# Kernel tuning notes

Measured on AMD Instinct MI355X. Metric: run time of the kernel, lower is better.

The kernel has to match this reference:

```python
import jax, jax.numpy as jnp
import numpy as np
import math

H = 8          # num_heads
DH = 16        # dim_head
DEPTH = 1
LAMBDA_INIT = 0.8 - 0.6 * math.exp(-0.3 * DEPTH)
LN_EPS = 1e-5


def setup_inputs() -> dict:
    key = jax.random.key(0)
    ks = jax.random.split(key, 12)
    dim = 256
    inner = 2 * H * DH  # 256
    b, n = 2, 2048
    s = lambda fan_in: 1.0 / math.sqrt(fan_in)
    return {
        "x": jax.random.normal(ks[0], (b, n, dim), jnp.float32),
        "Wq": jax.random.normal(ks[1], (dim, inner), jnp.float32) * s(dim),
        "Wkv": jax.random.normal(ks[2], (dim, 2 * inner), jnp.float32) * s(dim),
        "Wout": jax.random.normal(ks[3], (inner, dim), jnp.float32) * s(inner),
        "bout": jnp.zeros((dim,), jnp.float32),
        "Wg": jax.random.normal(ks[4], (dim, inner), jnp.float32) * s(dim),
        "bg": jnp.ones((inner,), jnp.float32),
        "lq1": jax.random.normal(ks[5], (DH,), jnp.float32) * 0.1,
        "lk1": jax.random.normal(ks[6], (DH,), jnp.float32) * 0.1,
        "lq2": jax.random.normal(ks[7], (DH,), jnp.float32) * 0.1,
        "lk2": jax.random.normal(ks[8], (DH,), jnp.float32) * 0.1,
        "ln_gamma": jnp.ones((2 * DH,), jnp.float32),
        "ln_beta": jnp.zeros((2 * DH,), jnp.float32),
    }


def reference(x, Wq, Wkv, Wout, bout, Wg, bg, lq1, lk1, lq2, lk2, ln_gamma, ln_beta):
    b, n, dim = x.shape
    scale = DH ** (-0.5)

    q = x @ Wq                                   # [b, n, 2*H*DH]
    kv = x @ Wkv                                 # [b, n, 4*H*DH]
    k, v = jnp.split(kv, 2, axis=-1)

    # doubled heads for q, k; normal heads with width 2*DH for v
    q = q.reshape(b, n, 2 * H, DH).transpose(0, 2, 1, 3) * scale  # [b, 2H, n, DH]
    k = k.reshape(b, n, 2 * H, DH).transpose(0, 2, 1, 3)          # [b, 2H, n, DH]
    v = v.reshape(b, n, H, 2 * DH).transpose(0, 2, 1, 3)          # [b, H, n, 2DH]

    dots = jnp.einsum('bhid,bhjd->bhij', q, k)   # [b, 2H, n, n]
    attn = jax.nn.softmax(dots, axis=-1)

    lam1 = jnp.exp(jnp.sum(lq1 * lk1))
    lam2 = jnp.exp(jnp.sum(lq2 * lk2))
    lam = lam1 - lam2 + LAMBDA_INIT

    attn = attn.reshape(b, H, 2, n, n)
    attn = attn[:, :, 0] - lam * attn[:, :, 1]   # [b, H, n, n]

    out = jnp.einsum('bhij,bhjd->bhid', attn, v)  # [b, H, n, 2DH]

    # LayerNorm over last dim (2*DH)
    mu = jnp.mean(out, axis=-1, keepdims=True)
    var = jnp.var(out, axis=-1, keepdims=True)
    out = (out - mu) * jax.lax.rsqrt(var + LN_EPS) * ln_gamma + ln_beta

    out = out * (1.0 - LAMBDA_INIT)
    out = out.transpose(0, 2, 1, 3).reshape(b, n, H * 2 * DH)  # [b, n, inner]

    gates = x @ Wg + bg
    out = out * jax.nn.sigmoid(gates)
    return out @ Wout + bout
```

## Files before the change

kernel.cpp:

```cpp
#include <hip/hip_runtime.h>
#include <hip/hip_bf16.h>

#define LAMBDA_INIT_F 0.35550906759096927f
#define ONE_MINUS_LI  0.64449093240903073f
#define QSCALE 0.36067376022224085f

typedef unsigned short u16;
typedef unsigned int   u32;
typedef short s8v  __attribute__((ext_vector_type(8)));
typedef u32   u32x4 __attribute__((ext_vector_type(4)));
typedef float f16v __attribute__((ext_vector_type(16)));

__device__ __forceinline__ u16 f2bf(float f) {
    __hip_bfloat16 h = __float2bfloat16(f);
    return *reinterpret_cast<u16*>(&h);
}
__device__ __forceinline__ u32 pk2bf(float lo, float hi) {
    return (u32)f2bf(lo) | ((u32)f2bf(hi) << 16);
}
union U4S8 { u32 u[4]; s8v s; };
__device__ __forceinline__ s8v mks8(u32 a, u32 b, u32 c, u32 d) {
    U4S8 x; x.u[0]=a; x.u[1]=b; x.u[2]=c; x.u[3]=d; return x.s;
}

__device__ __forceinline__ float fexp2(float x) {
#if __has_builtin(__builtin_amdgcn_exp2f)
    return __builtin_amdgcn_exp2f(x);
#else
    float r; asm volatile("v_exp_f32 %0, %1\n\ts_nop 1" : "=v"(r) : "v"(x)); return r;
#endif
}

#define MFMA16(a,b,c) __builtin_amdgcn_mfma_f32_32x32x16_bf16((a),(b),(c),0,0,0)

__device__ __forceinline__ void plswap2(u32& a, u32& b) {
    auto r = __builtin_amdgcn_permlane32_swap(a, b, false, false);
    a = r[0]; b = r[1];
}

__global__ __launch_bounds__(256) void prep_kernel(
    const float* __restrict__ Wq, const float* __restrict__ Wkv,
    const float* __restrict__ Wg, const float* __restrict__ Wout,
    const float* __restrict__ x,
    u16* __restrict__ WT, u16* __restrict__ xbf)
{
    const int bid = blockIdx.x;
    const int tid = threadIdx.x;

    if (bid >= 80) {
        const int r0 = (bid - 80) * 64;
        const float4* src = (const float4*)(x + (size_t)r0 * 256);
        u32* dst = (u32*)(xbf + (size_t)r0 * 256);
        for (int idx = tid; idx < 64 * 64; idx += 256) {
            float4 v = src[idx];
            dst[2*idx + 0] = pk2bf(v.x, v.y);
            dst[2*idx + 1] = pk2bf(v.z, v.w);
        }
        return;
    }

    __shared__ u16 tile[16 * 258];
    const int n0g = bid * 16;
    const float* src; int cols; int ncol0;
    if      (n0g < 256)  { src = Wq;   cols = 256; ncol0 = n0g; }
    else if (n0g < 768)  { src = Wkv;  cols = 512; ncol0 = n0g - 256; }
    else if (n0g < 1024) { src = Wg;   cols = 256; ncol0 = n0g - 768; }
    else                 { src = Wout; cols = 256; ncol0 = n0g - 1024; }

    const float* srow = src + (size_t)tid * cols + ncol0;
#pragma unroll
    for (int j = 0; j < 8; ++j) {
        const float2 v = *(const float2*)(srow + 2*j);
        tile[(2*j + 0) * 258 + tid] = f2bf(v.x);
        tile[(2*j + 1) * 258 + tid] = f2bf(v.y);
    }
    __syncthreads();

    const u32* t32 = (const u32*)tile;
    const int nn = tid >> 4, part = tid & 15;
    u32* dst = (u32*)WT + (size_t)(n0g + nn) * 128 + part * 8;
    const u32* s2 = t32 + nn * 129 + part * 8;
#pragma unroll
    for (int j = 0; j < 8; ++j) dst[j] = s2[j];
}

__global__ __launch_bounds__(256) void proj_kernel(
    const u16* __restrict__ x, const u16* __restrict__ WT,
    const float* __restrict__ bg,
    u16* __restrict__ Qb, u16* __restrict__ Kb,
    u16* __restrict__ Vb, float* __restrict__ Gb)
{
    const int bid = blockIdx.x;
    const int nt = bid & 15, mt = bid >> 4;
    const int tid = threadIdx.x, w = tid >> 6, lane = tid & 63;
    const int l31 = lane & 31, hh = lane >> 5;
    const int ms = w & 1, nsub = w >> 1;
    const int m0 = mt * 64 + ms * 32;
    const int n0 = nt * 64 + nsub * 32;

    const u16* xr = x  + (size_t)(m0 + l31) * 256 + 8*hh;
    const u16* br = WT + (size_t)(n0 + l31) * 256 + 8*hh;

    f16v a0;
#pragma unroll
    for (int r = 0; r < 16; ++r) a0[r] = 0.f;

#pragma unroll
    for (int ks = 0; ks < 16; ++ks) {
        s8v xa = *(const s8v*)(xr + ks*16);
        s8v w0 = *(const s8v*)(br + ks*16);
        a0 = MFMA16(xa, w0, a0);
    }

    const int cat = nt >> 2;
    const int n = n0 + l31;
#pragma unroll
    for (int r = 0; r < 16; ++r) {
        const int il = (r & 3) + 8*(r >> 2) + 4*hh;
        const int R = m0 + il;
        const int b = R >> 11, i = R & 2047;
        const float v = a0[r];
        if (cat == 0) {
            const int h = n >> 4, d = n & 15;
            Qb[((size_t)(b*16 + h) * 2048 + i) * 16 + d] = f2bf(v * QSCALE);
        } else if (cat == 1) {
            const int nk = n - 256, h = nk >> 4, d = nk & 15;
            Kb[((size_t)(b*16 + h) * 2048 + i) * 16 + d] = f2bf(v);
        } else if (cat == 2) {
            const int nv = n - 512, hv = nv >> 5, d2 = nv & 31;
            Vb[((size_t)(b*8 + hv) * 2048 + i) * 32 + d2] = f2bf(v);
        } else {
            const int gcol = n - 768;
            const float t = v + bg[gcol];
            Gb[(size_t)R * 256 + gcol] = 1.0f / (1.0f + __expf(-t));
        }
    }
}

__global__ __launch_bounds__(512, 8) void attn_kernel(
    const u16* __restrict__ Q, const u16* __restrict__ K,
    const u16* __restrict__ V, const float* __restrict__ G,
    const float* __restrict__ lq1, const float* __restrict__ lk1,
    const float* __restrict__ lq2, const float* __restrict__ lk2,
    const float* __restrict__ gamma, const float* __restrict__ beta,
    u16* __restrict__ A)
{
    __shared__ float smemf[8960];
    u16* st  = (u16*)smemf;
    u32* stu = (u32*)smemf;

    const int bid = blockIdx.x;
    const int itile = bid & 63;
    const int combo = bid >> 6;
    const int ho = combo & 7, b = combo >> 3;
    const int i0 = itile * 32;

    const int tid = threadIdx.x, w = tid >> 6, lane = tid & 63;
    const int l31 = lane & 31, hh = lane >> 5;
    const int s = w & 1, jq = w >> 1;

    const u16* Vg = V + (size_t)(b*8 + ho) * 2048 * 32;
    const u16* Qg = Q + ((size_t)(b*16 + 2*ho + s) * 2048 + (i0 + l31)) * 16;
    const s8v qf = *(const s8v*)(Qg + 8*hh);

    const int qp = tid >> 7;
    const int pid = tid & 127;
    const int ksub = pid >> 6, krow = (pid >> 1) & 31, kseg = pid & 1;
    const u32* kgp = (const u32*)(K + (size_t)(b*16 + 2*ho + ksub) * 2048 * 16)
                     + (size_t)qp * 4096 + krow * 8 + kseg * 4;
    const int vj = pid >> 2, vseg = pid & 3;
    const u32* vgp = (const u32*)Vg + (size_t)qp * 8192 + vj * 16 + vseg * 4;

    const int kw_off = qp*1120 + ksub*288 + krow*9 + kseg*4;
    const int vw_u16 = qp*2240 + 1152 + vj;
    const int vd0 = vseg * 8;
    const int kr_off = jq*1120 + s*288 + l31*9 + 4*hh;
    const int vr_off = jq*1120 + 576 + l31*17;

    f16v oacc;
#pragma unroll
    for (int r = 0; r < 16; ++r) oacc[r] = 0.f;
    float la0 = 0.f, la1 = 0.f;

    {
        u32 k0 = kgp[0], k1 = kgp[1], k2 = kgp[2], k3 = kgp[3];
        u32 v0 = vgp[0], v1 = vgp[1], v2 = vgp[2], v3 = vgp[3];
        u32* kd = stu + kw_off;
        kd[0]=k0; kd[1]=k1; kd[2]=k2; kd[3]=k3;
        u16* vd = st + vw_u16;
        vd[(vd0+0)*34] = (u16)(v0 & 0xffff); vd[(vd0+1)*34] = (u16)(v0 >> 16);
        vd[(vd0+2)*34] = (u16)(v1 & 0xffff); vd[(vd0+3)*34] = (u16)(v1 >> 16);
        vd[(vd0+4)*34] = (u16)(v2 & 0xffff); vd[(vd0+5)*34] = (u16)(v2 >> 16);
        vd[(vd0+6)*34] = (u16)(v3 & 0xffff); vd[(vd0+7)*34] = (u16)(v3 >> 16);
    }

    for (int t = 0; t < 16; ++t) {
        __syncthreads();
        const int p = t & 1, pn = 1 - p;
        const int tt = (t + 1) & 15;

        const u32* kp = kgp + (size_t)tt * 256;
        u32 nk0=kp[0], nk1=kp[1], nk2=kp[2], nk3=kp[3];
        const u32* vp = vgp + (size_t)tt * 512;
        u32 nv0=vp[0], nv1=vp[1], nv2=vp[2], nv3=vp[3];

        const u32* kb2 = stu + p*4480 + kr_off;
        const u32* vb2 = stu + p*4480 + vr_off;

        f16v sc;
#pragma unroll
        for (int r = 0; r < 16; ++r) sc[r] = 0.f;
        {
            s8v kf = mks8(kb2[0], kb2[1], kb2[2], kb2[3]);
            sc = MFMA16(kf, qf, sc);
        }
        float pv[16];
#pragma unroll
        for (int r = 0; r < 16; ++r) pv[r] = fexp2(sc[r]);
        la0 += pv[0];  la0 += pv[1];  la0 += pv[2];  la0 += pv[3];
        la1 += pv[4];  la1 += pv[5];  la1 += pv[6];  la1 += pv[7];
        la0 += pv[8];  la0 += pv[9];  la0 += pv[10]; la0 += pv[11];
        la1 += pv[12]; la1 += pv[13]; la1 += pv[14]; la1 += pv[15];

        u32 wv[8];
#pragma unroll
        for (int i = 0; i < 8; ++i)
            wv[i] = __builtin_amdgcn_perm(__float_as_uint(pv[2*i+1]),
                                          __float_as_uint(pv[2*i+0]), 0x07060302);
        plswap2(wv[0], wv[2]); plswap2(wv[1], wv[3]);
        {
            s8v pf0 = mks8(wv[0], wv[1], wv[2], wv[3]);
            s8v vf0 = mks8(vb2[4*hh+0], vb2[4*hh+1], vb2[4*hh+2], vb2[4*hh+3]);
            oacc = MFMA16(pf0, vf0, oacc);
        }
        plswap2(wv[4], wv[6]); plswap2(wv[5], wv[7]);
        {
            s8v pf1 = mks8(wv[4], wv[5], wv[6], wv[7]);
            s8v vf1 = mks8(vb2[8+4*hh+0], vb2[8+4*hh+1], vb2[8+4*hh+2], vb2[8+4*hh+3]);
            oacc = MFMA16(pf1, vf1, oacc);
        }

        {
            u32* kd = stu + pn*4480 + kw_off;
            kd[0]=nk0; kd[1]=nk1; kd[2]=nk2; kd[3]=nk3;
            u16* vd = st + pn*8960 + vw_u16;
            vd[(vd0+0)*34] = (u16)(nv0 & 0xffff); vd[(vd0+1)*34] = (u16)(nv0 >> 16);
            vd[(vd0+2)*34] = (u16)(nv1 & 0xffff); vd[(vd0+3)*34] = (u16)(nv1 >> 16);
            vd[(vd0+4)*34] = (u16)(nv2 & 0xffff); vd[(vd0+5)*34] = (u16)(nv2 >> 16);
            vd[(vd0+6)*34] = (u16)(nv3 & 0xffff); vd[(vd0+7)*34] = (u16)(nv3 >> 16);
        }
    }
    const float lacc = la0 + la1;

    __syncthreads();
    float ltot = lacc + __shfl_xor(lacc, 32);
    float* ob = smemf + w * 1056;
#pragma unroll
    for (int r = 0; r < 16; ++r) {
        const int il = (r & 3) + 8*(r >> 2) + 4*hh;
        ob[il*33 + l31] = oacc[r];
    }
    if (lane < 32) smemf[8448 + w*32 + l31] = ltot;
    __syncthreads();

    if (tid < 128) {
        const int ii = tid >> 2, sub = tid & 3, d0 = sub * 8;
        float l1 = 0.f, l2 = 0.f;
#pragma unroll
        for (int q = 0; q < 4; ++q) {
            l1 += smemf[8448 + (2*q + 0)*32 + ii];
            l2 += smemf[8448 + (2*q + 1)*32 + ii];
        }

        float sA = 0.f, sB = 0.f;
#pragma unroll
        for (int d = 0; d < 16; ++d) {
            sA += lq1[d] * lk1[d];
            sB += lq2[d] * lk2[d];
        }
        const float lam = __expf(sA) - __expf(sB) + LAMBDA_INIT_F;
        const float c1 = 1.f / l1, c2 = lam / l2;

        float od[8]; float mu = 0.f;
#pragma unroll
        for (int dd = 0; dd < 8; ++dd) {
            const int d = d0 + dd;
            float o1 = 0.f, o2 = 0.f;
#pragma unroll
            for (int q = 0; q < 4; ++q) {
                o1 += smemf[(2*q + 0)*1056 + ii*33 + d];
                o2 += smemf[(2*q + 1)*1056 + ii*33 + d];
            }
            od[dd] = o1 * c1 - o2 * c2;
            mu += od[dd];
        }
        mu += __shfl_xor(mu, 1); mu += __shfl_xor(mu, 2);
        mu *= (1.f / 32.f);
        float var = 0.f;
#pragma unroll
        for (int dd = 0; dd < 8; ++dd) { const float t2 = od[dd] - mu; var += t2 * t2; }
        var += __shfl_xor(var, 1); var += __shfl_xor(var, 2);
        var *= (1.f / 32.f);
        const float rs = rsqrtf(var + 1e-5f);

        const int R = b*2048 + i0 + ii;
        const float* Gr = G + (size_t)R * 256 + ho*32 + d0;
        const float4 g0 = *(const float4*)(Gr);
        const float4 g1 = *(const float4*)(Gr + 4);
        const float gg[8] = { g0.x, g0.y, g0.z, g0.w, g1.x, g1.y, g1.z, g1.w };
        float vals[8];
#pragma unroll
        for (int dd = 0; dd < 8; ++dd) {
            const float val = (od[dd] - mu)*rs*gamma[d0 + dd] + beta[d0 + dd];
            vals[dd] = val * ONE_MINUS_LI * gg[dd];
        }
        u32x4 pk;
        pk[0] = pk2bf(vals[0], vals[1]);
        pk[1] = pk2bf(vals[2], vals[3]);
        pk[2] = pk2bf(vals[4], vals[5]);
        pk[3] = pk2bf(vals[6], vals[7]);
        *reinterpret_cast<u32x4*>(A + (size_t)R * 256 + ho*32 + d0) = pk;
    }
}

__global__ __launch_bounds__(512) void out_kernel(
    const u16* __restrict__ Abf, const u16* __restrict__ WT,
    const float* __restrict__ bout, float* __restrict__ out)
{
    __shared__ float cs[4][32 * 33];

    const int bid = blockIdx.x;
    const int nt = bid & 3, mt = bid >> 2;
    const int tid = threadIdx.x, w = tid >> 6, lane = tid & 63;
    const int l31 = lane & 31, hh = lane >> 5;
    const int t = w >> 1, kh = w & 1;
    const int m0 = mt * 64 + (t & 1) * 32;
    const int n0 = nt * 64 + (t >> 1) * 32;

    const u16* ar = Abf + (size_t)(m0 + l31) * 256 + kh*128 + 8*hh;
    const u16* br = WT + (size_t)(1024 + n0 + l31) * 256 + kh*128 + 8*hh;

    f16v acc;
#pragma unroll
    for (int r = 0; r < 16; ++r) acc[r] = 0.f;

#pragma unroll
    for (int ks = 0; ks < 8; ++ks) {
        s8v aa = *(const s8v*)(ar + ks*16);
        s8v ba = *(const s8v*)(br + ks*16);
        acc = MFMA16(aa, ba, acc);
    }

    if (kh == 0) {
#pragma unroll
        for (int r = 0; r < 16; ++r) {
            const int il = (r & 3) + 8*(r >> 2) + 4*hh;
            cs[t][il*33 + l31] = acc[r];
        }
    }
    __syncthreads();
    if (kh == 1) {
        const float bv = bout[n0 + l31];
#pragma unroll
        for (int r = 0; r < 16; ++r) {
            const int il = (r & 3) + 8*(r >> 2) + 4*hh;
            const int m = m0 + il;
            out[(size_t)m * 256 + n0 + l31] = acc[r] + cs[t][il*33 + l31] + bv;
        }
    }
}

extern "C" void kernel_launch(void* const* d_in, const int* in_sizes, int n_in,
                              void* d_out, int out_size, void* d_ws, size_t ws_size,
                              hipStream_t stream) {
    const float* x    = (const float*)d_in[0];
    const float* Wq   = (const float*)d_in[1];
    const float* Wkv  = (const float*)d_in[2];
    const float* Wout = (const float*)d_in[3];
    const float* bout = (const float*)d_in[4];
    const float* Wg   = (const float*)d_in[5];
    const float* bg   = (const float*)d_in[6];
    const float* lq1  = (const float*)d_in[7];
    const float* lk1  = (const float*)d_in[8];
    const float* lq2  = (const float*)d_in[9];
    const float* lk2  = (const float*)d_in[10];
    const float* lng  = (const float*)d_in[11];
    const float* lnb  = (const float*)d_in[12];

    u16*   WT  = (u16*)d_ws;
    u16*   xbf = WT + 327680;
    u16*   Qb  = xbf + 1048576;
    u16*   Kb  = Qb + 1048576;
    u16*   Vb  = Kb + 1048576;
    float* Gb  = (float*)(Vb + 1048576);
    u16*   Abf = (u16*)(Gb + 1048576);

    hipLaunchKernelGGL(prep_kernel, dim3(144), dim3(256), 0, stream,
                       Wq, Wkv, Wg, Wout, x, WT, xbf);
    hipLaunchKernelGGL(proj_kernel, dim3(1024), dim3(256), 0, stream,
                       xbf, WT, bg, Qb, Kb, Vb, Gb);
    hipLaunchKernelGGL(attn_kernel, dim3(1024), dim3(512), 0, stream,
                       Qb, Kb, Vb, Gb, lq1, lk1, lq2, lk2, lng, lnb, Abf);
    hipLaunchKernelGGL(out_kernel, dim3(256), dim3(512), 0, stream,
                       Abf, WT, bout, (float*)d_out);
}
```

Baseline: 139.8 us.

## Store V transposed from projection kernel to avoid per-element LDS transpose

The projection kernel now writes V in a transposed [b,h,d,n] layout using packed bf16 pairs, so the attention kernel can load V tiles with vector 32-bit/64-bit LDS stores instead of scattering eight 16-bit values per thread. The shared-memory layout is re-padded (stride 1152 per quarter, row pitch 18) to fit the new V tile. This removes many narrow LDS writes per iteration in the inner loop, at the cost of strided global stores in the projection kernel and a slightly larger LDS footprint.

New measurement: 218.6 us. +56.3%, slower.

```diff
diff --git a/kernel.cpp b/kernel.cpp
--- a/kernel.cpp
+++ b/kernel.cpp
@@ -8,6 +8,7 @@
 typedef unsigned short u16;
 typedef unsigned int   u32;
 typedef short s8v  __attribute__((ext_vector_type(8)));
+typedef u32   u32x2 __attribute__((ext_vector_type(2)));
 typedef u32   u32x4 __attribute__((ext_vector_type(4)));
 typedef float f16v __attribute__((ext_vector_type(16)));
 
@@ -114,25 +115,36 @@
 
     const int cat = nt >> 2;
     const int n = n0 + l31;
-#pragma unroll
-    for (int r = 0; r < 16; ++r) {
-        const int il = (r & 3) + 8*(r >> 2) + 4*hh;
-        const int R = m0 + il;
-        const int b = R >> 11, i = R & 2047;
-        const float v = a0[r];
-        if (cat == 0) {
-            const int h = n >> 4, d = n & 15;
-            Qb[((size_t)(b*16 + h) * 2048 + i) * 16 + d] = f2bf(v * QSCALE);
-        } else if (cat == 1) {
-            const int nk = n - 256, h = nk >> 4, d = nk & 15;
-            Kb[((size_t)(b*16 + h) * 2048 + i) * 16 + d] = f2bf(v);
-        } else if (cat == 2) {
-            const int nv = n - 512, hv = nv >> 5, d2 = nv & 31;
-            Vb[((size_t)(b*8 + hv) * 2048 + i) * 32 + d2] = f2bf(v);
-        } else {
-            const int gcol = n - 768;
-            const float t = v + bg[gcol];
-            Gb[(size_t)R * 256 + gcol] = 1.0f / (1.0f + __expf(-t));
+    if (cat == 2) {
+        const int nv = n - 512, hv = nv >> 5, d2 = nv & 31;
+#pragma unroll
+        for (int g = 0; g < 4; ++g) {
+            const int R0 = m0 + 8*g + 4*hh;
+            const int b = R0 >> 11, i = R0 & 2047;
+            u32x2 vv;
+            vv[0] = pk2bf(a0[4*g + 0], a0[4*g + 1]);
+            vv[1] = pk2bf(a0[4*g + 2], a0[4*g + 3]);
+            *reinterpret_cast<u32x2*>(
+                (u32*)Vb + ((size_t)(b*8 + hv) * 32 + d2) * 1024 + (i >> 1)) = vv;
+        }
+    } else {
+#pragma unroll
+        for (int r = 0; r < 16; ++r) {
+            const int il = (r & 3) + 8*(r >> 2) + 4*hh;
+            const int R = m0 + il;
+            const int b = R >> 11, i = R & 2047;
+            const float v = a0[r];
+            if (cat == 0) {
+                const int h = n >> 4, d = n & 15;
+                Qb[((size_t)(b*16 + h) * 2048 + i) * 16 + d] = f2bf(v * QSCALE);
+            } else if (cat == 1) {
+                const int nk = n - 256, h = nk >> 4, d = nk & 15;
+                Kb[((size_t)(b*16 + h) * 2048 + i) * 16 + d] = f2bf(v);
+            } else {
+                const int gcol = n - 768;
+                const float t = v + bg[gcol];
+                Gb[(size_t)R * 256 + gcol] = 1.0f / (1.0f + __expf(-t));
+            }
         }
     }
 }
@@ -145,8 +157,7 @@
     const float* __restrict__ gamma, const float* __restrict__ beta,
     u16* __restrict__ A)
 {
-    __shared__ float smemf[8960];
-    u16* st  = (u16*)smemf;
+    __shared__ float smemf[9216];
     u32* stu = (u32*)smemf;
 
     const int bid = blockIdx.x;
@@ -159,7 +170,6 @@
     const int l31 = lane & 31, hh = lane >> 5;
     const int s = w & 1, jq = w >> 1;
 
-    const u16* Vg = V + (size_t)(b*8 + ho) * 2048 * 32;
     const u16* Qg = Q + ((size_t)(b*16 + 2*ho + s) * 2048 + (i0 + l31)) * 16;
     const s8v qf = *(const s8v*)(Qg + 8*hh);
 
@@ -168,14 +178,14 @@
     const int ksub = pid >> 6, krow = (pid >> 1) & 31, kseg = pid & 1;
     const u32* kgp = (const u32*)(K + (size_t)(b*16 + 2*ho + ksub) * 2048 * 16)
                      + (size_t)qp * 4096 + krow * 8 + kseg * 4;
-    const int vj = pid >> 2, vseg = pid & 3;
-    const u32* vgp = (const u32*)Vg + (size_t)qp * 8192 + vj * 16 + vseg * 4;
-
-    const int kw_off = qp*1120 + ksub*288 + krow*9 + kseg*4;
-    const int vw_u16 = qp*2240 + 1152 + vj;
-    const int vd0 = vseg * 8;
-    const int kr_off = jq*1120 + s*288 + l31*9 + 4*hh;
-    const int vr_off = jq*1120 + 576 + l31*17;
+    const int vd = pid >> 2, jseg = pid & 3;
+    const u32* vgp = (const u32*)V + (size_t)(b*8 + ho) * 32768
+                     + vd * 1024 + qp * 256 + jseg * 4;
+
+    const int kw_off = qp*1152 + ksub*288 + krow*9 + kseg*4;
+    const int vw_off = qp*1152 + 576 + vd*18 + jseg*4;
+    const int kr_off = jq*1152 + s*288 + l31*9 + 4*hh;
+    const int vr_off = jq*1152 + 576 + l31*18;
 
     f16v oacc;
 #pragma unroll
@@ -187,11 +197,11 @@
         u32 v0 = vgp[0], v1 = vgp[1], v2 = vgp[2], v3 = vgp[3];
         u32* kd = stu + kw_off;
         kd[0]=k0; kd[1]=k1; kd[2]=k2; kd[3]=k3;
-        u16* vd = st + vw_u16;
-        vd[(vd0+0)*34] = (u16)(v0 & 0xffff); vd[(vd0+1)*34] = (u16)(v0 >> 16);
-        vd[(vd0+2)*34] = (u16)(v1 & 0xffff); vd[(vd0+3)*34] = (u16)(v1 >> 16);
-        vd[(vd0+4)*34] = (u16)(v2 & 0xffff); vd[(vd0+5)*34] = (u16)(v2 >> 16);
-        vd[(vd0+6)*34] = (u16)(v3 & 0xffff); vd[(vd0+7)*34] = (u16)(v3 >> 16);
+        u32* vdst = stu + vw_off;
+        u32x2 va; va[0]=v0; va[1]=v1;
+        u32x2 vb2w; vb2w[0]=v2; vb2w[1]=v3;
+        *reinterpret_cast<u32x2*>(vdst) = va;
+        *reinterpret_cast<u32x2*>(vdst + 2) = vb2w;
     }
 
     for (int t = 0; t < 16; ++t) {
@@ -201,11 +211,11 @@
 
         const u32* kp = kgp + (size_t)tt * 256;
         u32 nk0=kp[0], nk1=kp[1], nk2=kp[2], nk3=kp[3];
-        const u32* vp = vgp + (size_t)tt * 512;
+        const u32* vp = vgp + (size_t)tt * 16;
         u32 nv0=vp[0], nv1=vp[1], nv2=vp[2], nv3=vp[3];
 
-        const u32* kb2 = stu + p*4480 + kr_off;
-        const u32* vb2 = stu + p*4480 + vr_off;
+        const u32* kb2 = stu + p*4608 + kr_off;
+        const u32* vb2 = stu + p*4608 + vr_off;
 
         f16v sc;
 #pragma unroll
@@ -241,13 +251,13 @@
         }
 
         {
-            u32* kd = stu + pn*4480 + kw_off;
+            u32* kd = stu + pn*4608 + kw_off;
             kd[0]=nk0; kd[1]=nk1; kd[2]=nk2; kd[3]=nk3;
-            u16* vd = st + pn*8960 + vw_u16;
-            vd[(vd0+0)*34] = (u16)(nv0 & 0xffff); vd[(vd0+1)*34] = (u16)(nv0 >> 16);
-            vd[(vd0+2)*34] = (u16)(nv1 & 0xffff); vd[(vd0+3)*34] = (u16)(nv1 >> 16);
-            vd[(vd0+4)*34] = (u16)(nv2 & 0xffff); vd[(vd0+5)*34] = (u16)(nv2 >> 16);
-            vd[(vd0+6)*34] = (u16)(nv3 & 0xffff); vd[(vd0+7)*34] = (u16)(nv3 >> 16);
+            u32* vdst = stu + pn*4608 + vw_off;
+            u32x2 va; va[0]=nv0; va[1]=nv1;
+            u32x2 vb2w; vb2w[0]=nv2; vb2w[1]=nv3;
+            *reinterpret_cast<u32x2*>(vdst) = va;
+            *reinterpret_cast<u32x2*>(vdst + 2) = vb2w;
         }
     }
     const float lacc = la0 + la1;
```

## Swizzle block indices across XCDs and split out_kernel into smaller split-K tiles

Applied to the files above, without the earlier changes.

Adds an XCD-aware block-index remap in the proj, attn and out kernels, so blocks that share operands are grouped onto the same chiplet and its L2 cache. Restructures the output GEMM from 256 blocks of 64x64 tiles into 1024 blocks of 32x32 tiles. Each block now splits K four ways across its waves and reduces the partial sums through shared memory. The aim is better L2 locality and more parallelism in the small final GEMM, at the cost of extra LDS traffic for the reduction.

Measured after the change: 142.4 us. Within noise of the previous version (+1.9%).

```diff
diff --git a/kernel.cpp b/kernel.cpp
--- a/kernel.cpp
+++ b/kernel.cpp
@@ -36,6 +36,10 @@
 __device__ __forceinline__ void plswap2(u32& a, u32& b) {
     auto r = __builtin_amdgcn_permlane32_swap(a, b, false, false);
     a = r[0]; b = r[1];
+}
+
+__device__ __forceinline__ int xcd_swz1024(int bid) {
+    return (bid & 7) * 128 + (bid >> 3);
 }
 
 __global__ __launch_bounds__(256) void prep_kernel(
@@ -90,8 +94,8 @@
     u16* __restrict__ Qb, u16* __restrict__ Kb,
     u16* __restrict__ Vb, float* __restrict__ Gb)
 {
-    const int bid = blockIdx.x;
-    const int nt = bid & 15, mt = bid >> 4;
+    const int bidl = xcd_swz1024(blockIdx.x);
+    const int nt = bidl & 15, mt = bidl >> 4;
     const int tid = threadIdx.x, w = tid >> 6, lane = tid & 63;
     const int l31 = lane & 31, hh = lane >> 5;
     const int ms = w & 1, nsub = w >> 1;
@@ -149,9 +153,9 @@
     u16* st  = (u16*)smemf;
     u32* stu = (u32*)smemf;
 
-    const int bid = blockIdx.x;
-    const int itile = bid & 63;
-    const int combo = bid >> 6;
+    const int bidl = xcd_swz1024(blockIdx.x);
+    const int itile = bidl & 63;
+    const int combo = bidl >> 6;
     const int ho = combo & 7, b = combo >> 3;
     const int i0 = itile * 32;
 
@@ -323,50 +327,47 @@
     }
 }
 
-__global__ __launch_bounds__(512) void out_kernel(
+__global__ __launch_bounds__(256) void out_kernel(
     const u16* __restrict__ Abf, const u16* __restrict__ WT,
     const float* __restrict__ bout, float* __restrict__ out)
 {
     __shared__ float cs[4][32 * 33];
 
-    const int bid = blockIdx.x;
-    const int nt = bid & 3, mt = bid >> 2;
+    const int bidl = xcd_swz1024(blockIdx.x);
+    const int mt = bidl >> 3, nt = bidl & 7;
     const int tid = threadIdx.x, w = tid >> 6, lane = tid & 63;
     const int l31 = lane & 31, hh = lane >> 5;
-    const int t = w >> 1, kh = w & 1;
-    const int m0 = mt * 64 + (t & 1) * 32;
-    const int n0 = nt * 64 + (t >> 1) * 32;
-
-    const u16* ar = Abf + (size_t)(m0 + l31) * 256 + kh*128 + 8*hh;
-    const u16* br = WT + (size_t)(1024 + n0 + l31) * 256 + kh*128 + 8*hh;
+    const int m0 = mt * 32;
+    const int n0 = nt * 32;
+
+    const u16* ar = Abf + (size_t)(m0 + l31) * 256 + w*64 + 8*hh;
+    const u16* br = WT + (size_t)(1024 + n0 + l31) * 256 + w*64 + 8*hh;
 
     f16v acc;
 #pragma unroll
     for (int r = 0; r < 16; ++r) acc[r] = 0.f;
 
 #pragma unroll
-    for (int ks = 0; ks < 8; ++ks) {
+    for (int ks = 0; ks < 4; ++ks) {
         s8v aa = *(const s8v*)(ar + ks*16);
         s8v ba = *(const s8v*)(br + ks*16);
         acc = MFMA16(aa, ba, acc);
     }
 
-    if (kh == 0) {
-#pragma unroll
-        for (int r = 0; r < 16; ++r) {
-            const int il = (r & 3) + 8*(r >> 2) + 4*hh;
-            cs[t][il*33 + l31] = acc[r];
-        }
+#pragma unroll
+    for (int r = 0; r < 16; ++r) {
+        const int il = (r & 3) + 8*(r >> 2) + 4*hh;
+        cs[w][il*33 + l31] = acc[r];
     }
     __syncthreads();
-    if (kh == 1) {
-        const float bv = bout[n0 + l31];
-#pragma unroll
-        for (int r = 0; r < 16; ++r) {
-            const int il = (r & 3) + 8*(r >> 2) + 4*hh;
-            const int m = m0 + il;
-            out[(size_t)m * 256 + n0 + l31] = acc[r] + cs[t][il*33 + l31] + bv;
-        }
+
+#pragma unroll
+    for (int e = 0; e < 4; ++e) {
+        const int idx = tid + e*256;
+        const int m = idx >> 5, nn = idx & 31;
+        const float val = cs[0][m*33 + nn] + cs[1][m*33 + nn]
+                        + cs[2][m*33 + nn] + cs[3][m*33 + nn] + bout[n0 + nn];
+        out[(size_t)(m0 + m) * 256 + n0 + nn] = val;
     }
 }
 
@@ -401,6 +402,6 @@
                        xbf, WT, bg, Qb, Kb, Vb, Gb);
     hipLaunchKernelGGL(attn_kernel, dim3(1024), dim3(512), 0, stream,
                        Qb, Kb, Vb, Gb, lq1, lk1, lq2, lk2, lng, lnb, Abf);
-    hipLaunchKernelGGL(out_kernel, dim3(256), dim3(512), 0, stream,
+    hipLaunchKernelGGL(out_kernel, dim3(1024), dim3(256), 0, stream,
                        Abf, WT, bout, (float*)d_out);
 }
```
